# Kernel tuning notes

Hardware: AMD Instinct MI355X
Metric: run time of the kernel (lower is better)

## Reference

```python
import jax, jax.numpy as jnp
import numpy as np

BIG = 1e10  # sentinel depth for empty pixels


def setup_inputs() -> dict:
    key = jax.random.key(0)
    k1, k2, k3, k4, k5 = jax.random.split(key, 5)
    N, C = 200000, 64
    B, H, W = 4, 376, 1241
    features = jax.random.normal(k1, (N, C), dtype=jnp.float32)
    # coordinates: [batch_id, z, y, x]; grid is ~67 bins per axis given
    # voxel_size=0.75 and pcd_range [0,-25,-25,50,25,25]
    b = jax.random.randint(k2, (N, 1), 0, B, dtype=jnp.int32)
    z = jax.random.randint(k3, (N, 1), 0, 67, dtype=jnp.int32)
    y = jax.random.randint(k4, (N, 1), 0, 67, dtype=jnp.int32)
    x = jax.random.randint(k5, (N, 1), 0, 67, dtype=jnp.int32)
    coordinates = jnp.concatenate([b, z, y, x], axis=1)
    # KITTI-like pinhole intrinsics
    K = jnp.array([[721.5377, 0.0, 609.5593],
                   [0.0, 721.5377, 172.854],
                   [0.0, 0.0, 1.0]], dtype=jnp.float32)
    return {"features": features, "coordinates": coordinates, "K": K,
            "batch_size": B, "h": H, "w": W}


def _projection_matrix(K):
    # module-constant R and V2P (from __init__ defaults)
    R = jnp.array([[0., -1., 0.], [0., 0., -1.], [1., 0., 0.]], dtype=jnp.float32)
    vx = vy = vz = 0.75
    x_off = vx / 2 + 0.0
    y_off = vy / 2 + (-25.0)
    z_off = vz / 2 + (-25.0)
    V2P = jnp.array([[vx, 0., 0., x_off],
                     [0., vy, 0., y_off],
                     [0., 0., vz, z_off]], dtype=jnp.float32)
    return K @ R @ V2P  # [3,4]


def reference(features, coordinates, K, batch_size, h, w):
    N, C = features.shape
    P = _projection_matrix(K)  # [3,4]
    b = coordinates[:, 0]
    # coordinates order is [batch_id, z, y, x]; homogeneous point is [x,y,z,1]
    xyz1 = jnp.stack([coordinates[:, 3], coordinates[:, 2], coordinates[:, 1],
                      jnp.ones_like(coordinates[:, 0])], axis=1).astype(jnp.float32)
    p = xyz1 @ P.T  # [N,3]
    depth = p[:, 2]
    safe_d = jnp.where(depth > 1e-6, depth, 1.0)
    u = jnp.floor(p[:, 0] / safe_d).astype(jnp.int32)
    v = jnp.floor(p[:, 1] / safe_d).astype(jnp.int32)
    valid = (depth > 1e-6) & (u >= 0) & (u < w) & (v >= 0) & (v < h)
    num_pix = batch_size * h * w
    pix = jnp.where(valid, b * (h * w) + v * w + u, 0)
    d = jnp.where(valid, depth, BIG)
    # z-buffer: min depth per pixel, then winning voxel index (tie -> smallest idx)
    min_depth = jnp.full((num_pix,), BIG, dtype=jnp.float32).at[pix].min(d)
    is_win = valid & (d <= min_depth[pix])
    cand = jnp.where(is_win, jnp.arange(N, dtype=jnp.int32), N)
    win_idx = jnp.full((num_pix,), N, dtype=jnp.int32).at[pix].min(cand)
    feats_pad = jnp.concatenate([features, jnp.zeros((1, C), features.dtype)], axis=0)
    out = feats_pad[win_idx].reshape(batch_size, h, w, C).transpose(0, 3, 1, 2)  # [B,C,H,W]
    inv_depth = jnp.where(min_depth < BIG, 1.0 / min_depth, 0.0).reshape(batch_size, h, w)
    return out, inv_depth
```

## Files before the change

kernel.cpp:

```cpp
#include <hip/hip_runtime.h>
#include <cstdint>
#include <cstddef>

constexpr int Bc = 4;
constexpr int Hc = 376;
constexpr int Wc = 1241;
constexpr int Cc = 64;
constexpr int HW = Hc * Wc;
constexpr int NUM_PIX = Bc * HW;


__global__ void init_entries(uint4* __restrict__ p, int n16) {
    int t = blockIdx.x * blockDim.x + threadIdx.x;
    if (t < n16) p[t] = make_uint4(0xFFFFFFFFu, 0xFFFFFFFFu, 0xFFFFFFFFu, 0xFFFFFFFFu);
}

__global__ void scatter_points(const int* __restrict__ coords,
                               const float* __restrict__ Km,
                               unsigned long long* __restrict__ entries,
                               int N) {
    int n = blockIdx.x * blockDim.x + threadIdx.x;
    if (n >= N) return;

    const int4 co = *(const int4*)(coords + 4 * (size_t)n);
    const int   bi = co.x;
    const float zf = (float)co.y;
    const float yf = (float)co.z;
    const float xf = (float)co.w;

    float P0[4], P1[4], P2[4];
    {
        const float xo = 0.375f, yo = -24.625f, zo = -24.625f;
        float KR0, KR1, KR2;
        KR0 = Km[2]; KR1 = -Km[0]; KR2 = -Km[1];
        P0[0] = __fmaf_rn(KR0, 0.75f, 0.0f);
        P0[1] = __fmaf_rn(KR1, 0.75f, 0.0f);
        P0[2] = __fmaf_rn(KR2, 0.75f, 0.0f);
        P0[3] = __fmaf_rn(KR2, zo, __fmaf_rn(KR1, yo, __fmaf_rn(KR0, xo, 0.0f)));
        KR0 = Km[5]; KR1 = -Km[3]; KR2 = -Km[4];
        P1[0] = __fmaf_rn(KR0, 0.75f, 0.0f);
        P1[1] = __fmaf_rn(KR1, 0.75f, 0.0f);
        P1[2] = __fmaf_rn(KR2, 0.75f, 0.0f);
        P1[3] = __fmaf_rn(KR2, zo, __fmaf_rn(KR1, yo, __fmaf_rn(KR0, xo, 0.0f)));
        KR0 = Km[8]; KR1 = -Km[6]; KR2 = -Km[7];
        P2[0] = __fmaf_rn(KR0, 0.75f, 0.0f);
        P2[1] = __fmaf_rn(KR1, 0.75f, 0.0f);
        P2[2] = __fmaf_rn(KR2, 0.75f, 0.0f);
        P2[3] = __fmaf_rn(KR2, zo, __fmaf_rn(KR1, yo, __fmaf_rn(KR0, xo, 0.0f)));
    }

    float p0 = __fmaf_rn(1.0f, P0[3], __fmaf_rn(zf, P0[2], __fmaf_rn(yf, P0[1], __fmaf_rn(xf, P0[0], 0.0f))));
    float p1 = __fmaf_rn(1.0f, P1[3], __fmaf_rn(zf, P1[2], __fmaf_rn(yf, P1[1], __fmaf_rn(xf, P1[0], 0.0f))));
    float depth = __fmaf_rn(1.0f, P2[3], __fmaf_rn(zf, P2[2], __fmaf_rn(yf, P2[1], __fmaf_rn(xf, P2[0], 0.0f))));

    const bool dok = depth > 1e-6f;
    const float safe_d = dok ? depth : 1.0f;
    const int u = (int)floorf(__fdiv_rn(p0, safe_d));
    const int v = (int)floorf(__fdiv_rn(p1, safe_d));

    if (dok && u >= 0 && u < Wc && v >= 0 && v < Hc && bi >= 0 && bi < Bc) {
        const int pix = bi * HW + v * Wc + u;
        const unsigned long long key =
            ((unsigned long long)__float_as_uint(depth) << 32) | (unsigned int)n;
        atomicMin(&entries[pix], key);
    }
}

__global__ void decode_entries(const unsigned long long* __restrict__ entries,
                               int* __restrict__ widx,
                               float* __restrict__ inv_depth) {
    int t = blockIdx.x * blockDim.x + threadIdx.x;
    if (t >= NUM_PIX) return;
    const unsigned long long e = entries[t];
    int idx = -1;
    float inv = 0.0f;
    if (e != ~0ULL) {
        idx = (int)(unsigned int)(e & 0xFFFFFFFFu);
        const float dep = __uint_as_float((unsigned int)(e >> 32));
        inv = __fdiv_rn(1.0f, dep);
    }
    widx[t] = idx;
    inv_depth[t] = inv;
}

__global__ void gather_features(const int* __restrict__ widx,
                                const float* __restrict__ feat,
                                float* __restrict__ out) {
    const int q = blockIdx.x * blockDim.x + threadIdx.x;
    if (q >= HW / 4) return;
    const int c = blockIdx.y;
    const int b = blockIdx.z;
    const int local = q * 4;

    const int4 i4 = *(const int4*)(widx + (size_t)b * HW + local);
    float4 o;
    o.x = (i4.x < 0) ? 0.0f : feat[(size_t)i4.x * Cc + c];
    o.y = (i4.y < 0) ? 0.0f : feat[(size_t)i4.y * Cc + c];
    o.z = (i4.z < 0) ? 0.0f : feat[(size_t)i4.z * Cc + c];
    o.w = (i4.w < 0) ? 0.0f : feat[(size_t)i4.w * Cc + c];

    *(float4*)(out + ((size_t)(b * Cc + c) * HW + local)) = o;
}

extern "C" void kernel_launch(void* const* d_in, const int* in_sizes, int n_in,
                              void* d_out, int out_size, void* d_ws, size_t ws_size,
                              hipStream_t stream) {
    const float* features = (const float*)d_in[0];
    const int*   coords   = (const int*)d_in[1];
    const float* Km       = (const float*)d_in[2];
    const int N = in_sizes[1] / 4;

    unsigned long long* entries = (unsigned long long*)d_ws;
    int* widx = (int*)((char*)d_ws + (size_t)NUM_PIX * 8);

    float* out_feat = (float*)d_out;
    float* out_inv  = (float*)d_out + (size_t)Bc * Cc * HW;

    const int n16 = NUM_PIX / 2;
    init_entries<<<(n16 + 255) / 256, 256, 0, stream>>>((uint4*)entries, n16);

    scatter_points<<<(N + 255) / 256, 256, 0, stream>>>(coords, Km, entries, N);

    decode_entries<<<(NUM_PIX + 255) / 256, 256, 0, stream>>>(entries, widx, out_inv);

    dim3 ggrid((HW / 4 + 255) / 256, Cc, Bc);
    gather_features<<<ggrid, 256, 0, stream>>>(widx, features, out_feat);
}
```

Measured before the change: 525.8 us.

## Fuse decode and feature gather into tiled shared-memory transpose kernel

Merges the decode kernel and the per-channel gather kernel into one kernel. Each block handles 64 pixels: it decodes the z-buffer entries, reads whole 256-byte feature rows with coalesced float4 loads, transposes them through padded shared memory, and writes the channel-major output. This removes the intermediate index buffer and the 64 separate gathers of scattered single floats per pixel. In exchange each output store is only 64 floats per channel row (256 bytes), and the 16 KB shared tile per block may limit occupancy.

```diff
diff --git a/kernel.cpp b/kernel.cpp
--- a/kernel.cpp
+++ b/kernel.cpp
@@ -8,6 +8,9 @@
 constexpr int Cc = 64;
 constexpr int HW = Hc * Wc;
 constexpr int NUM_PIX = Bc * HW;
+constexpr int TILE = 64;
+constexpr int PAD = 65;
+constexpr int NTILES = (NUM_PIX + TILE - 1) / TILE;
 
 
 __global__ void init_entries(uint4* __restrict__ p, int n16) {
@@ -66,40 +69,56 @@
     }
 }
 
-__global__ void decode_entries(const unsigned long long* __restrict__ entries,
-                               int* __restrict__ widx,
-                               float* __restrict__ inv_depth) {
-    int t = blockIdx.x * blockDim.x + threadIdx.x;
-    if (t >= NUM_PIX) return;
-    const unsigned long long e = entries[t];
-    int idx = -1;
-    float inv = 0.0f;
-    if (e != ~0ULL) {
-        idx = (int)(unsigned int)(e & 0xFFFFFFFFu);
-        const float dep = __uint_as_float((unsigned int)(e >> 32));
-        inv = __fdiv_rn(1.0f, dep);
+__global__ __launch_bounds__(256, 2)
+void gather_tile(const unsigned long long* __restrict__ entries,
+                 const float* __restrict__ feat,
+                 float* __restrict__ out_feat,
+                 float* __restrict__ out_inv) {
+    __shared__ float smem[TILE * PAD];
+    __shared__ int   s_idx[TILE];
+
+    const int tid  = threadIdx.x;
+    const int wave = tid >> 6;
+    const int lane = tid & 63;
+    const int g0   = blockIdx.x * TILE;
+
+    if (tid < TILE) {
+        int idx = -1;
+        if (g0 + tid < NUM_PIX) {
+            const unsigned long long e = entries[g0 + tid];
+            float inv = 0.0f;
+            if (e != ~0ULL) {
+                idx = (int)(unsigned int)(e & 0xFFFFFFFFu);
+                inv = __fdiv_rn(1.0f, __uint_as_float((unsigned int)(e >> 32)));
+            }
+            out_inv[g0 + tid] = inv;
+        }
+        s_idx[tid] = idx;
     }
-    widx[t] = idx;
-    inv_depth[t] = inv;
-}
+    __syncthreads();
 
-__global__ void gather_features(const int* __restrict__ widx,
-                                const float* __restrict__ feat,
-                                float* __restrict__ out) {
-    const int q = blockIdx.x * blockDim.x + threadIdx.x;
-    if (q >= HW / 4) return;
-    const int c = blockIdx.y;
-    const int b = blockIdx.z;
-    const int local = q * 4;
+    const float4* feat4 = (const float4*)feat;
+    const int j = lane & 15;
+    for (int it = 0; it < 4; ++it) {
+        const int p = (wave * 4 + it) * 4 + (lane >> 4);
+        const int idx = s_idx[p];
+        float4 v = make_float4(0.f, 0.f, 0.f, 0.f);
+        if (idx >= 0) v = feat4[(size_t)idx * 16 + j];
+        float* row = smem + p * PAD + 4 * j;
+        row[0] = v.x; row[1] = v.y; row[2] = v.z; row[3] = v.w;
+    }
+    __syncthreads();
 
-    const int4 i4 = *(const int4*)(widx + (size_t)b * HW + local);
-    float4 o;
-    o.x = (i4.x < 0) ? 0.0f : feat[(size_t)i4.x * Cc + c];
-    o.y = (i4.y < 0) ? 0.0f : feat[(size_t)i4.y * Cc + c];
-    o.z = (i4.z < 0) ? 0.0f : feat[(size_t)i4.z * Cc + c];
-    o.w = (i4.w < 0) ? 0.0f : feat[(size_t)i4.w * Cc + c];
-
-    *(float4*)(out + ((size_t)(b * Cc + c) * HW + local)) = o;
+    const int g = g0 + lane;
+    if (g < NUM_PIX) {
+        const int b = g / HW;
+        const int local = g - b * HW;
+        float* outBase = out_feat + (size_t)b * Cc * HW + local;
+        for (int i = 0; i < 16; ++i) {
+            const int c = wave * 16 + i;
+            outBase[(size_t)c * HW] = smem[lane * PAD + c];
+        }
+    }
 }
 
 extern "C" void kernel_launch(void* const* d_in, const int* in_sizes, int n_in,
@@ -111,7 +130,6 @@
     const int N = in_sizes[1] / 4;
 
     unsigned long long* entries = (unsigned long long*)d_ws;
-    int* widx = (int*)((char*)d_ws + (size_t)NUM_PIX * 8);
 
     float* out_feat = (float*)d_out;
     float* out_inv  = (float*)d_out + (size_t)Bc * Cc * HW;
@@ -121,8 +139,5 @@
 
     scatter_points<<<(N + 255) / 256, 256, 0, stream>>>(coords, Km, entries, N);
 
-    decode_entries<<<(NUM_PIX + 255) / 256, 256, 0, stream>>>(entries, widx, out_inv);
-
-    dim3 ggrid((HW / 4 + 255) / 256, Cc, Bc);
-    gather_features<<<ggrid, 256, 0, stream>>>(widx, features, out_feat);
+    gather_tile<<<NTILES, 256, 0, stream>>>(entries, features, out_feat, out_inv);
 }
```

New measurement: 586.7 us. 11.6% more time.

## Fuse decode and feature gather into one per-pixel row-gather kernel

Applied to the files above, without the earlier changes.

The separate decode and per-channel gather kernels are merged into one kernel where each thread handles one pixel. The thread decodes the z-buffer entry, writes the inverse depth, loads the winning voxel's full 64-float feature row as float4s, and writes it out channel by channel with stride HW. This drops the intermediate index buffer and one launch, and reads each feature row once instead of 64 scattered times. In exchange each thread holds 64 floats in registers, and every store is a scalar store, coalesced across threads but no longer vectorised.

```diff
diff --git a/kernel.cpp b/kernel.cpp
--- a/kernel.cpp
+++ b/kernel.cpp
@@ -66,40 +66,37 @@
     }
 }
 
-__global__ void decode_entries(const unsigned long long* __restrict__ entries,
-                               int* __restrict__ widx,
-                               float* __restrict__ inv_depth) {
-    int t = blockIdx.x * blockDim.x + threadIdx.x;
-    if (t >= NUM_PIX) return;
-    const unsigned long long e = entries[t];
-    int idx = -1;
+__global__ void gather_rows(const unsigned long long* __restrict__ entries,
+                            const float* __restrict__ feat,
+                            float* __restrict__ out_feat,
+                            float* __restrict__ out_inv) {
+    const int g = blockIdx.x * blockDim.x + threadIdx.x;
+    if (g >= NUM_PIX) return;
+
+    const unsigned long long e = entries[g];
+
+    float4 row[16];
+    #pragma unroll
+    for (int k = 0; k < 16; ++k) row[k] = make_float4(0.f, 0.f, 0.f, 0.f);
+
     float inv = 0.0f;
     if (e != ~0ULL) {
-        idx = (int)(unsigned int)(e & 0xFFFFFFFFu);
-        const float dep = __uint_as_float((unsigned int)(e >> 32));
-        inv = __fdiv_rn(1.0f, dep);
+        const int idx = (int)(unsigned int)(e & 0xFFFFFFFFu);
+        inv = __fdiv_rn(1.0f, __uint_as_float((unsigned int)(e >> 32)));
+        const float4* fr = (const float4*)(feat + (size_t)idx * Cc);
+        #pragma unroll
+        for (int k = 0; k < 16; ++k) row[k] = fr[k];
     }
-    widx[t] = idx;
-    inv_depth[t] = inv;
-}
+    out_inv[g] = inv;
 
-__global__ void gather_features(const int* __restrict__ widx,
-                                const float* __restrict__ feat,
-                                float* __restrict__ out) {
-    const int q = blockIdx.x * blockDim.x + threadIdx.x;
-    if (q >= HW / 4) return;
-    const int c = blockIdx.y;
-    const int b = blockIdx.z;
-    const int local = q * 4;
-
-    const int4 i4 = *(const int4*)(widx + (size_t)b * HW + local);
-    float4 o;
-    o.x = (i4.x < 0) ? 0.0f : feat[(size_t)i4.x * Cc + c];
-    o.y = (i4.y < 0) ? 0.0f : feat[(size_t)i4.y * Cc + c];
-    o.z = (i4.z < 0) ? 0.0f : feat[(size_t)i4.z * Cc + c];
-    o.w = (i4.w < 0) ? 0.0f : feat[(size_t)i4.w * Cc + c];
-
-    *(float4*)(out + ((size_t)(b * Cc + c) * HW + local)) = o;
+    const int b = g / HW;
+    const int local = g - b * HW;
+    float* o = out_feat + (size_t)b * Cc * HW + local;
+    const float* r = (const float*)row;
+    #pragma unroll
+    for (int c = 0; c < Cc; ++c) {
+        o[(size_t)c * HW] = r[c];
+    }
 }
 
 extern "C" void kernel_launch(void* const* d_in, const int* in_sizes, int n_in,
@@ -111,7 +108,6 @@
     const int N = in_sizes[1] / 4;
 
     unsigned long long* entries = (unsigned long long*)d_ws;
-    int* widx = (int*)((char*)d_ws + (size_t)NUM_PIX * 8);
 
     float* out_feat = (float*)d_out;
     float* out_inv  = (float*)d_out + (size_t)Bc * Cc * HW;
@@ -121,8 +117,5 @@
 
     scatter_points<<<(N + 255) / 256, 256, 0, stream>>>(coords, Km, entries, N);
 
-    decode_entries<<<(NUM_PIX + 255) / 256, 256, 0, stream>>>(entries, widx, out_inv);
-
-    dim3 ggrid((HW / 4 + 255) / 256, Cc, Bc);
-    gather_features<<<ggrid, 256, 0, stream>>>(widx, features, out_feat);
+    gather_rows<<<(NUM_PIX + 255) / 256, 256, 0, stream>>>(entries, features, out_feat, out_inv);
 }
```

Measured after the change: 566.6 us. 1.08x slower.
